# Performance work log

Hardware: AMD Instinct MI355X
Metric: run time of the kernel (lower is better)

## Reference

```python
import jax, jax.numpy as jnp
import numpy as np

B, S, HID = 2, 2048, 2048
NH, NKV, D = 16, 4, 128  # heads, kv heads, dim_per_head
ROPE_BASE = 10000.0


def setup_inputs() -> dict:
    key = jax.random.key(0)
    ks = jax.random.split(key, 5)
    x = jax.random.normal(ks[0], (B, S, HID), jnp.float32)
    wq = jax.random.normal(ks[1], (HID, NH * D), jnp.float32) * 0.02
    wk = jax.random.normal(ks[2], (HID, NKV * D), jnp.float32) * 0.02
    wv = jax.random.normal(ks[3], (HID, NKV * D), jnp.float32) * 0.02
    wo = jax.random.normal(ks[4], (NH * D, HID), jnp.float32) * 0.02
    inv_freq = 1.0 / (ROPE_BASE ** (jnp.arange(0, D, 2, dtype=jnp.float32) / D))
    freqs = jnp.outer(jnp.arange(S, dtype=jnp.float32), inv_freq)  # [S, D/2]
    cos, sin = jnp.cos(freqs), jnp.sin(freqs)
    mask = jnp.tril(jnp.ones((S, S), dtype=bool))  # causal, True = attend
    return {"x": x, "wq": wq, "wk": wk, "wv": wv, "wo": wo,
            "cos": cos, "sin": sin, "mask": mask}


def _rope_interleave(t, cos, sin):
    # t: [B, H, S, D]; cos/sin: [S, D/2]; interleaved pairs (even, odd)
    te, to = t[..., ::2], t[..., 1::2]
    c, s = cos[None, None], sin[None, None]
    re = te * c - to * s
    ro = to * c + te * s
    return jnp.stack([re, ro], axis=-1).reshape(t.shape)


def reference(x, wq, wk, wv, wo, cos, sin, mask):
    b, s, _ = x.shape
    # QKV projections + shape(): [B, S, hid] -> [B, H, S, D]
    q = (x @ wq).reshape(b, s, NH, D).transpose(0, 2, 1, 3)
    k = (x @ wk).reshape(b, s, NKV, D).transpose(0, 2, 1, 3)
    v = (x @ wv).reshape(b, s, NKV, D).transpose(0, 2, 1, 3)
    q = _rope_interleave(q, cos, sin)
    k = _rope_interleave(k, cos, sin)
    # GQA: repeat each kv head heads//heads_kv times consecutively
    rep = NH // NKV
    k = jnp.repeat(k, rep, axis=1)
    v = jnp.repeat(v, rep, axis=1)
    scores = jnp.einsum('bhqd,bhkd->bhqk', q, k) * (D ** -0.5)
    scores = scores.astype(jnp.float32)
    scores = jnp.where(mask[None, None], scores, jnp.finfo(jnp.float32).min)
    attn = jax.nn.softmax(scores, axis=-1).astype(x.dtype)
    ctx = jnp.einsum('bhqk,bhkd->bhqd', attn, v)
    ctx = ctx.transpose(0, 2, 1, 3).reshape(b, s, NH * D)  # unshape()
    return ctx @ wo
```

## Files before the change

### kernel.cpp

```cpp
#include <hip/hip_runtime.h>
#include <hip/hip_bf16.h>
#include <math.h>

#define S_LEN 2048
#define HIDW 2048
#define NHEAD 16
#define NKVH 4
#define HD 128
#define NB 2
#define MROWS (NB * S_LEN)
#define QKVN (NHEAD * HD + 2 * NKVH * HD)
#define KOFF (NHEAD * HD)
#define VOFF (NHEAD * HD + NKVH * HD)

typedef __bf16 bf16_t;
typedef __bf16 bf16x4_t __attribute__((ext_vector_type(4)));
typedef __bf16 bf16x8_t __attribute__((ext_vector_type(8)));
typedef float f32x4_t __attribute__((ext_vector_type(4)));

__device__ __forceinline__ void gload_lds16(const bf16_t* g, bf16_t* l) {
  __builtin_amdgcn_global_load_lds(
      (const __attribute__((address_space(1))) void*)g,
      (__attribute__((address_space(3))) void*)l, 16, 0, 0);
}

__device__ __forceinline__ f32x4_t zero4() {
  f32x4_t z = {0.f, 0.f, 0.f, 0.f};
  return z;
}

__device__ __forceinline__ float fexp2(float x) {
#if __has_builtin(__builtin_amdgcn_exp2f)
  return __builtin_amdgcn_exp2f(x);
#else
  return exp2f(x);
#endif
}

__global__ __launch_bounds__(256) void k_cvt8(const float* __restrict__ in,
                                              bf16_t* __restrict__ out, int n8) {
  int i = blockIdx.x * 256 + threadIdx.x;
  if (i >= n8) return;
  const float4* p = (const float4*)(in + (size_t)i * 8);
  float4 a = p[0], b = p[1];
  bf16x8_t r;
  r[0] = (bf16_t)a.x; r[1] = (bf16_t)a.y; r[2] = (bf16_t)a.z; r[3] = (bf16_t)a.w;
  r[4] = (bf16_t)b.x; r[5] = (bf16_t)b.y; r[6] = (bf16_t)b.z; r[7] = (bf16_t)b.w;
  *(bf16x8_t*)(out + (size_t)i * 8) = r;
}

__global__ __launch_bounds__(256) void k_tr_cvt(const float* __restrict__ in,
                                                bf16_t* __restrict__ out, int R, int C) {
  __shared__ float t[32][33];
  int c0 = blockIdx.x * 32, r0 = blockIdx.y * 32;
  int tx = threadIdx.x & 31, ty = threadIdx.x >> 5;
#pragma unroll
  for (int rr = ty; rr < 32; rr += 8) t[rr][tx] = in[(size_t)(r0 + rr) * C + c0 + tx];
  __syncthreads();
#pragma unroll
  for (int rr = ty; rr < 32; rr += 8)
    out[(size_t)(c0 + rr) * R + r0 + tx] = (bf16_t)t[tx][rr];
}

template <int EPI, int BMH>
__global__ __launch_bounds__(512, 2) void k_gemm256(const bf16_t* __restrict__ A,
                                                    const bf16_t* __restrict__ Bt,
                                                    void* __restrict__ Cout,
                                                    int M, int N, int K, int nby,
                                                    const float* __restrict__ cosT,
                                                    const float* __restrict__ sinT) {
  __shared__ bf16_t As[2][BMH * 128 * 64];
  __shared__ bf16_t Bs[2][256 * 64];

  int tid = threadIdx.x;
  int lane = tid & 63, wid = tid >> 6;
  int l15 = lane & 15, lg = lane >> 4;
  int wrb = (wid >> 2) * (BMH * 64);
  int wcb = (wid & 3) * 64;

  int nwg = gridDim.x;
  int qx = nwg >> 3;
  int lin = blockIdx.x;
  int wg = (lin & 7) * qx + (lin >> 3);
  int row0 = (wg / nby) * (BMH * 128), col0 = (wg % nby) * 256;

  int srow = tid >> 3;
  int scol = ((tid & 7) ^ (srow & 7)) * 8;
  const bf16_t* Ag = A + (size_t)(row0 + srow) * K + scol;
  const bf16_t* Bg = Bt + (size_t)(col0 + srow) * K + scol;

  f32x4_t acc[BMH * 4][4];
#pragma unroll
  for (int i = 0; i < BMH * 4; i++)
#pragma unroll
    for (int j = 0; j < 4; j++) acc[i][j] = zero4();

  int xr = (l15 & 7) << 4;
  int nk = K >> 6;

  auto stA = [&](int tt, int u) {
    gload_lds16(Ag + (size_t)u * 64 * K + (size_t)tt * 64,
                As[tt & 1] + u * 4096 + tid * 8);
  };
  auto stB = [&](int tt, int u) {
    gload_lds16(Bg + (size_t)u * 64 * K + (size_t)tt * 64,
                Bs[tt & 1] + u * 4096 + tid * 8);
  };

  for (int tt = 0; tt < 2 && tt < nk; tt++) {
    for (int u = 0; u < BMH * 2; u++) stA(tt, u);
    for (int u = 0; u < 4; u++) stB(tt, u);
  }
  if (nk > 1) {
    if constexpr (BMH == 2) asm volatile("s_waitcnt vmcnt(8)" ::: "memory");
    else asm volatile("s_waitcnt vmcnt(6)" ::: "memory");
  } else {
    asm volatile("s_waitcnt vmcnt(0)" ::: "memory");
  }
  __builtin_amdgcn_s_barrier();
  __builtin_amdgcn_sched_barrier(0);

  for (int t = 0; t < nk; t++) {
    int cur = t & 1;
    const char* Ac = (const char*)As[cur];
    const char* Bc = (const char*)Bs[cur];
    bool pf = (t + 2 < nk);

    bf16x8_t af0[4][2], bfr[4][2];
#pragma unroll
    for (int i = 0; i < 4; i++) {
      int row = wrb + i * 16 + l15;
#pragma unroll
      for (int kk = 0; kk < 2; kk++)
        af0[i][kk] = *(const bf16x8_t*)(Ac + ((row * 128 + kk * 64 + lg * 16) ^ xr));
    }
#pragma unroll
    for (int jn = 0; jn < 4; jn++) {
      int rowb = wcb + jn * 16 + l15;
#pragma unroll
      for (int kk = 0; kk < 2; kk++)
        bfr[jn][kk] = *(const bf16x8_t*)(Bc + ((rowb * 128 + kk * 64 + lg * 16) ^ xr));
    }
    __builtin_amdgcn_s_barrier();
    __builtin_amdgcn_s_setprio(1);
    if constexpr (BMH == 2) {
#pragma unroll
      for (int i = 0; i < 4; i++)
#pragma unroll
        for (int j = 0; j < 2; j++)
#pragma unroll
          for (int kk = 0; kk < 2; kk++)
            acc[i][j] = __builtin_amdgcn_mfma_f32_16x16x32_bf16(af0[i][kk], bfr[j][kk],
                                                                acc[i][j], 0, 0, 0);
    } else {
#pragma unroll
      for (int i = 0; i < 4; i++)
#pragma unroll
        for (int kk = 0; kk < 2; kk++)
          acc[i][0] = __builtin_amdgcn_mfma_f32_16x16x32_bf16(af0[i][kk], bfr[0][kk],
                                                              acc[i][0], 0, 0, 0);
    }
    __builtin_amdgcn_s_setprio(0);

    if (pf) {
      stA(t + 2, 0);
      if constexpr (BMH == 2) stA(t + 2, 2);
      else stA(t + 2, 1);
    }
    __builtin_amdgcn_s_barrier();
    __builtin_amdgcn_s_setprio(1);
    if constexpr (BMH == 2) {
#pragma unroll
      for (int i = 0; i < 4; i++)
#pragma unroll
        for (int j = 0; j < 2; j++)
#pragma unroll
          for (int kk = 0; kk < 2; kk++)
            acc[i][2 + j] = __builtin_amdgcn_mfma_f32_16x16x32_bf16(
                af0[i][kk], bfr[2 + j][kk], acc[i][2 + j], 0, 0, 0);
    } else {
#pragma unroll
      for (int i = 0; i < 4; i++)
#pragma unroll
        for (int kk = 0; kk < 2; kk++)
          acc[i][1] = __builtin_amdgcn_mfma_f32_16x16x32_bf16(af0[i][kk], bfr[1][kk],
                                                              acc[i][1], 0, 0, 0);
    }
    __builtin_amdgcn_s_setprio(0);

    bf16x8_t af1[4][2];
    if constexpr (BMH == 2) {
#pragma unroll
      for (int i = 0; i < 4; i++) {
        int row = wrb + 64 + i * 16 + l15;
#pragma unroll
        for (int kk = 0; kk < 2; kk++)
          af1[i][kk] = *(const bf16x8_t*)(Ac + ((row * 128 + kk * 64 + lg * 16) ^ xr));
      }
    }
    if (pf) { stB(t + 2, 0); stB(t + 2, 1); }
    __builtin_amdgcn_s_barrier();
    __builtin_amdgcn_s_setprio(1);
    if constexpr (BMH == 2) {
#pragma unroll
      for (int i = 0; i < 4; i++)
#pragma unroll
        for (int j = 0; j < 2; j++)
#pragma unroll
          for (int kk = 0; kk < 2; kk++)
            acc[4 + i][j] = __builtin_amdgcn_mfma_f32_16x16x32_bf16(
                af1[i][kk], bfr[j][kk], acc[4 + i][j], 0, 0, 0);
    } else {
#pragma unroll
      for (int i = 0; i < 4; i++)
#pragma unroll
        for (int kk = 0; kk < 2; kk++)
          acc[i][2] = __builtin_amdgcn_mfma_f32_16x16x32_bf16(af0[i][kk], bfr[2][kk],
                                                              acc[i][2], 0, 0, 0);
    }
    __builtin_amdgcn_s_setprio(0);

    if (pf) {
      stB(t + 2, 2); stB(t + 2, 3);
      if constexpr (BMH == 2) { stA(t + 2, 1); stA(t + 2, 3); }
    }
    __builtin_amdgcn_s_barrier();
    __builtin_amdgcn_s_setprio(1);
    if constexpr (BMH == 2) {
#pragma unroll
      for (int i = 0; i < 4; i++)
#pragma unroll
        for (int j = 0; j < 2; j++)
#pragma unroll
          for (int kk = 0; kk < 2; kk++)
            acc[4 + i][2 + j] = __builtin_amdgcn_mfma_f32_16x16x32_bf16(
                af1[i][kk], bfr[2 + j][kk], acc[4 + i][2 + j], 0, 0, 0);
    } else {
#pragma unroll
      for (int i = 0; i < 4; i++)
#pragma unroll
        for (int kk = 0; kk < 2; kk++)
          acc[i][3] = __builtin_amdgcn_mfma_f32_16x16x32_bf16(af0[i][kk], bfr[3][kk],
                                                              acc[i][3], 0, 0, 0);
    }
    __builtin_amdgcn_s_setprio(0);

    if (t + 1 < nk) {
      if (pf) {
        if constexpr (BMH == 2) asm volatile("s_waitcnt vmcnt(8)" ::: "memory");
        else asm volatile("s_waitcnt vmcnt(6)" ::: "memory");
      } else {
        asm volatile("s_waitcnt vmcnt(0)" ::: "memory");
      }
    }
    __builtin_amdgcn_s_barrier();
    __builtin_amdgcn_sched_barrier(0);
  }

  if (EPI == 2) {
    if (col0 < VOFF) {
      int sbase = row0 & (S_LEN - 1);
      bf16_t* cosL = &As[0][0];
      bf16_t* sinL = &Bs[0][0];
#pragma unroll
      for (int k = 0; k < 8; k++) {
        gload_lds16((const bf16_t*)(cosT + (size_t)sbase * 64 + k * 2048 + tid * 4),
                    cosL + k * 4096 + tid * 8);
        gload_lds16((const bf16_t*)(sinT + (size_t)sbase * 64 + k * 2048 + tid * 4),
                    sinL + k * 4096 + tid * 8);
      }
      asm volatile("s_waitcnt vmcnt(0)" ::: "memory");
      __builtin_amdgcn_s_barrier();
      const float* cosF = (const float*)cosL;
      const float* sinF = (const float*)sinL;
      const float QS = 0.08838834764831845f * 1.4426950408889634f;
#pragma unroll
      for (int i = 0; i < BMH * 4; i++) {
#pragma unroll
        for (int j = 0; j < 4; j++) {
          int c = col0 + wcb + j * 16 + l15;
          int rlb = wrb + i * 16 + lg * 4;
          float scale = (c < KOFF) ? QS : 1.0f;
          int p0 = (c & 127) >> 1;
          int codd = c & 1;
#pragma unroll
          for (int qd = 0; qd < 4; qd++) {
            int rl = rlb + qd;
            float self = acc[i][j][qd];
            float other = __shfl_xor(self, 1);
            float cv = cosF[rl * 64 + p0], sv = sinF[rl * 64 + p0];
            float outv = codd ? (self * cv + other * sv) : (self * cv - other * sv);
            ((bf16_t*)Cout)[(size_t)(row0 + rl) * N + c] = (bf16_t)(outv * scale);
          }
        }
      }
    } else {
#pragma unroll
      for (int i = 0; i < BMH * 4; i++) {
#pragma unroll
        for (int j = 0; j < 4; j++) {
          int r = row0 + wrb + i * 16 + lg * 4;
          int c = col0 + wcb + j * 16 + l15;
#pragma unroll
          for (int qd = 0; qd < 4; qd++)
            ((bf16_t*)Cout)[(size_t)(r + qd) * N + c] = (bf16_t)acc[i][j][qd];
        }
      }
    }
  } else {
#pragma unroll
    for (int i = 0; i < BMH * 4; i++) {
#pragma unroll
      for (int j = 0; j < 4; j++) {
        int r = row0 + wrb + i * 16 + lg * 4;
        int c = col0 + wcb + j * 16 + l15;
#pragma unroll
        for (int qd = 0; qd < 4; qd++)
          ((float*)Cout)[(size_t)(r + qd) * N + c] = acc[i][j][qd];
      }
    }
  }
}

__global__ __launch_bounds__(256) void k_vt(const bf16_t* __restrict__ qkv,
                                            bf16_t* __restrict__ vt) {
  __shared__ bf16_t t[32][33];
  int s0 = blockIdx.x * 32;
  int dt = (blockIdx.y & 3) * 32;
  int h = blockIdx.y >> 2;
  int b = blockIdx.z;
  int tx = threadIdx.x & 31, ty = threadIdx.x >> 5;
#pragma unroll
  for (int rr = ty; rr < 32; rr += 8)
    t[rr][tx] = qkv[(size_t)(b * S_LEN + s0 + rr) * QKVN + VOFF + h * HD + dt + tx];
  __syncthreads();
#pragma unroll
  for (int rr = ty; rr < 32; rr += 8)
    vt[((size_t)((b * NKVH + h) * HD + dt + rr)) * S_LEN + s0 + tx] = t[tx][rr];
}

__global__ __launch_bounds__(256, 2) void k_attn(const bf16_t* __restrict__ qkv,
                                                 const bf16_t* __restrict__ vt,
                                                 bf16_t* __restrict__ ctx) {
  __shared__ bf16_t Ks[2 * 64 * 128];
  __shared__ bf16_t Vs[2 * 128 * 64];
  __shared__ bf16_t plds[4][16 * 72];

  int tid = threadIdx.x;
  int lane = tid & 63, wid = tid >> 6;
  int idx = blockIdx.x;
  int bh = idx & 31;
  int qg = 31 - (idx >> 5);
  int b = bh >> 4, h = bh & 15;
  int kvh = h >> 2;
  int q0 = qg * 64 + wid * 16;
  int l15 = lane & 15, lg = lane >> 4;

  const bf16_t* Kbase = qkv + (size_t)(b * S_LEN) * QKVN + KOFF + kvh * HD;
  const bf16_t* Vbase = vt + (size_t)(b * NKVH + kvh) * HD * S_LEN;

  const bf16_t* Qp = qkv + (size_t)(b * S_LEN + q0 + l15) * QKVN + h * HD + lg * 8;
  bf16x8_t aq[4];
#pragma unroll
  for (int kk = 0; kk < 4; kk++) aq[kk] = *(const bf16x8_t*)(Qp + kk * 32);

  int Ls[4], Lk[4], Lv[4];
#pragma unroll
  for (int u = 0; u < 4; u++) {
    int L = u * 4096 + tid * 16;
    Ls[u] = L >> 1;
    Lk[u] = L ^ (((L >> 8) & 7) << 4);
    Lv[u] = L ^ (((L >> 7) & 7) << 4);
  }

  f32x4_t o[8];
#pragma unroll
  for (int j = 0; j < 8; j++) o[j] = zero4();
  float ms = -INFINITY, lsum = 0.f;

  bf16_t* pbuf = &plds[wid][0];
  int xr = (l15 & 7) << 4;
  int ntiles = qg + 1;
  int qcol = q0 + l15;

#pragma unroll
  for (int u = 0; u < 4; u++) {
    gload_lds16(Kbase + (size_t)(Lk[u] >> 8) * QKVN + ((Lk[u] & 255) >> 1), Ks + Ls[u]);
    gload_lds16(Vbase + (size_t)(Lv[u] >> 7) * S_LEN + ((Lv[u] & 127) >> 1), Vs + Ls[u]);
  }
  __syncthreads();

  for (int t = 0; t < ntiles; t++) {
    int kv0 = t * 64;
    if (t + 1 < ntiles) {
      const bf16_t* Kn = Kbase + (size_t)(kv0 + 64) * QKVN;
      const bf16_t* Vn = Vbase + kv0 + 64;
      int bo = ((t + 1) & 1) * 8192;
#pragma unroll
      for (int u = 0; u < 4; u++) {
        gload_lds16(Kn + (size_t)(Lk[u] >> 8) * QKVN + ((Lk[u] & 255) >> 1), Ks + bo + Ls[u]);
        gload_lds16(Vn + (size_t)(Lv[u] >> 7) * S_LEN + ((Lv[u] & 127) >> 1), Vs + bo + Ls[u]);
      }
    }
    const char* Kb = (const char*)Ks + (t & 1) * 16384;
    const char* Vb = (const char*)Vs + (t & 1) * 16384;

    f32x4_t sacc[4];
#pragma unroll
    for (int cg = 0; cg < 4; cg++) sacc[cg] = zero4();
#pragma unroll
    for (int cg = 0; cg < 4; cg++) {
#pragma unroll
      for (int kk = 0; kk < 4; kk++) {
        int boff = ((cg * 16 + l15) * 256 + kk * 64 + lg * 16) ^ xr;
        bf16x8_t bk = *(const bf16x8_t*)(Kb + boff);
        sacc[cg] = __builtin_amdgcn_mfma_f32_16x16x32_bf16(bk, aq[kk], sacc[cg], 0, 0, 0);
      }
    }
    if (kv0 + 63 > q0) {
#pragma unroll
      for (int cg = 0; cg < 4; cg++) {
#pragma unroll
        for (int i = 0; i < 4; i++) {
          int kvg = kv0 + cg * 16 + lg * 4 + i;
          if (kvg > qcol) sacc[cg][i] = -1e30f;
        }
      }
    }
    float pmax = sacc[0][0];
#pragma unroll
    for (int cg = 0; cg < 4; cg++)
#pragma unroll
      for (int i = 0; i < 4; i++) pmax = fmaxf(pmax, sacc[cg][i]);
    pmax = fmaxf(pmax, __shfl_xor(pmax, 16));
    pmax = fmaxf(pmax, __shfl_xor(pmax, 32));
    if (__any(pmax - ms > 8.0f)) {
      float nm = fmaxf(ms, pmax);
      float sc = fexp2(ms - nm);
      ms = nm;
      lsum *= sc;
      float sci[4];
#pragma unroll
      for (int i = 0; i < 4; i++) sci[i] = __shfl(sc, lg * 4 + i);
#pragma unroll
      for (int j = 0; j < 8; j++)
#pragma unroll
        for (int i = 0; i < 4; i++) o[j][i] *= sci[i];
    }
    float ls = 0.f;
#pragma unroll
    for (int cg = 0; cg < 4; cg++)
#pragma unroll
      for (int i = 0; i < 4; i++) {
        sacc[cg][i] = fexp2(sacc[cg][i] - ms);
        ls += sacc[cg][i];
      }
    ls += __shfl_xor(ls, 16);
    ls += __shfl_xor(ls, 32);
    lsum += ls;
#pragma unroll
    for (int cg = 0; cg < 4; cg++)
#pragma unroll
      for (int i = 0; i < 4; i++)
        pbuf[l15 * 72 + cg * 16 + lg * 4 + i] = (bf16_t)sacc[cg][i];
    __builtin_amdgcn_wave_barrier();
    bf16x8_t pa0 = *(const bf16x8_t*)(pbuf + l15 * 72 + lg * 8);
    bf16x8_t pa1 = *(const bf16x8_t*)(pbuf + l15 * 72 + 32 + lg * 8);
    __builtin_amdgcn_wave_barrier();
#pragma unroll
    for (int j = 0; j < 8; j++) {
      int d = j * 16 + l15;
      int bo0 = (d * 128 + lg * 16) ^ xr;
      int bo1 = (d * 128 + 64 + lg * 16) ^ xr;
      o[j] = __builtin_amdgcn_mfma_f32_16x16x32_bf16(
          pa0, *(const bf16x8_t*)(Vb + bo0), o[j], 0, 0, 0);
      o[j] = __builtin_amdgcn_mfma_f32_16x16x32_bf16(
          pa1, *(const bf16x8_t*)(Vb + bo1), o[j], 0, 0, 0);
    }
    __syncthreads();
  }

  bf16_t* Cp = ctx + (size_t)(b * S_LEN + q0) * KOFF + h * HD;
#pragma unroll
  for (int i = 0; i < 4; i++) {
    float inv = 1.f / __shfl(lsum, lg * 4 + i);
    int row = lg * 4 + i;
#pragma unroll
    for (int j = 0; j < 8; j++)
      Cp[(size_t)row * KOFF + j * 16 + l15] = (bf16_t)(o[j][i] * inv);
  }
}

extern "C" void kernel_launch(void* const* d_in, const int* in_sizes, int n_in,
                              void* d_out, int out_size, void* d_ws, size_t ws_size,
                              hipStream_t stream) {
  const float* x = (const float*)d_in[0];
  const float* wq = (const float*)d_in[1];
  const float* wk = (const float*)d_in[2];
  const float* wv = (const float*)d_in[3];
  const float* wo = (const float*)d_in[4];
  const float* cosT = (const float*)d_in[5];
  const float* sinT = (const float*)d_in[6];

  bf16_t* xb = (bf16_t*)d_ws;
  bf16_t* wqkvT = xb + (size_t)MROWS * HIDW;
  bf16_t* woT = wqkvT + (size_t)QKVN * HIDW;
  bf16_t* qkv = woT + (size_t)HIDW * HIDW;
  bf16_t* vtb = qkv + (size_t)MROWS * QKVN;

  k_cvt8<<<MROWS * HIDW / 8 / 256, 256, 0, stream>>>(x, xb, MROWS * HIDW / 8);
  k_tr_cvt<<<dim3(KOFF / 32, HIDW / 32), 256, 0, stream>>>(wq, wqkvT, HIDW, KOFF);
  k_tr_cvt<<<dim3((NKVH * HD) / 32, HIDW / 32), 256, 0, stream>>>(
      wk, wqkvT + (size_t)KOFF * HIDW, HIDW, NKVH * HD);
  k_tr_cvt<<<dim3((NKVH * HD) / 32, HIDW / 32), 256, 0, stream>>>(
      wv, wqkvT + (size_t)VOFF * HIDW, HIDW, NKVH * HD);
  k_tr_cvt<<<dim3(HIDW / 32, KOFF / 32), 256, 0, stream>>>(wo, woT, KOFF, HIDW);
  k_gemm256<2, 2><<<(MROWS / 256) * (QKVN / 256), 512, 0, stream>>>(
      xb, wqkvT, qkv, MROWS, QKVN, HIDW, QKVN / 256, cosT, sinT);
  k_vt<<<dim3(S_LEN / 32, 4 * NKVH, NB), 256, 0, stream>>>(qkv, vtb);
  k_attn<<<32 * 32, 256, 0, stream>>>(qkv, vtb, xb);
  k_gemm256<0, 1><<<(MROWS / 128) * (HIDW / 256), 512, 0, stream>>>(
      xb, woT, d_out, MROWS, HIDW, KOFF, HIDW / 256, nullptr, nullptr);
}
```

Before: 193.9 us.

## Simplify GEMM mainloop to single-stage prefetch with one barrier per tile

Replaces the depth-two prefetch, whose global-to-LDS loads were interleaved between four barrier-separated MFMA phases, with a simpler depth-one scheme. All loads for the next K tile are issued at the top of each iteration into the other LDS buffer, and the loop waits with vmcnt(0) plus one barrier at the end. B fragments are now read from LDS in two halves just before they are used, which lowers register pressure and removes three barriers per iteration. In exchange there is less latency hiding, because only one tile is in flight and every iteration fully drains outstanding memory loads. The sched_barrier hints are also removed, leaving scheduling to the compiler.

New measurement: 214.6 us. +10.7%, slower.

```diff
diff --git a/kernel.cpp b/kernel.cpp
--- a/kernel.cpp
+++ b/kernel.cpp
@@ -107,26 +107,22 @@
                 Bs[tt & 1] + u * 4096 + tid * 8);
   };
 
-  for (int tt = 0; tt < 2 && tt < nk; tt++) {
-    for (int u = 0; u < BMH * 2; u++) stA(tt, u);
-    for (int u = 0; u < 4; u++) stB(tt, u);
-  }
-  if (nk > 1) {
-    if constexpr (BMH == 2) asm volatile("s_waitcnt vmcnt(8)" ::: "memory");
-    else asm volatile("s_waitcnt vmcnt(6)" ::: "memory");
-  } else {
-    asm volatile("s_waitcnt vmcnt(0)" ::: "memory");
-  }
+  for (int u = 0; u < BMH * 2; u++) stA(0, u);
+  for (int u = 0; u < 4; u++) stB(0, u);
+  asm volatile("s_waitcnt vmcnt(0)" ::: "memory");
   __builtin_amdgcn_s_barrier();
-  __builtin_amdgcn_sched_barrier(0);
 
   for (int t = 0; t < nk; t++) {
-    int cur = t & 1;
-    const char* Ac = (const char*)As[cur];
-    const char* Bc = (const char*)Bs[cur];
-    bool pf = (t + 2 < nk);
-
-    bf16x8_t af0[4][2], bfr[4][2];
+    const char* Ac = (const char*)As[t & 1];
+    const char* Bc = (const char*)Bs[t & 1];
+    if (t + 1 < nk) {
+#pragma unroll
+      for (int u = 0; u < BMH * 2; u++) stA(t + 1, u);
+#pragma unroll
+      for (int u = 0; u < 4; u++) stB(t + 1, u);
+    }
+
+    bf16x8_t af0[4][2], b01[2][2];
 #pragma unroll
     for (int i = 0; i < 4; i++) {
       int row = wrb + i * 16 + l15;
@@ -135,61 +131,44 @@
         af0[i][kk] = *(const bf16x8_t*)(Ac + ((row * 128 + kk * 64 + lg * 16) ^ xr));
     }
 #pragma unroll
-    for (int jn = 0; jn < 4; jn++) {
-      int rowb = wcb + jn * 16 + l15;
+    for (int j = 0; j < 2; j++) {
+      int rowb = wcb + j * 16 + l15;
 #pragma unroll
       for (int kk = 0; kk < 2; kk++)
-        bfr[jn][kk] = *(const bf16x8_t*)(Bc + ((rowb * 128 + kk * 64 + lg * 16) ^ xr));
-    }
-    __builtin_amdgcn_s_barrier();
+        b01[j][kk] = *(const bf16x8_t*)(Bc + ((rowb * 128 + kk * 64 + lg * 16) ^ xr));
+    }
     __builtin_amdgcn_s_setprio(1);
+#pragma unroll
+    for (int i = 0; i < 4; i++)
+#pragma unroll
+      for (int j = 0; j < 2; j++)
+#pragma unroll
+        for (int kk = 0; kk < 2; kk++)
+          acc[i][j] = __builtin_amdgcn_mfma_f32_16x16x32_bf16(af0[i][kk], b01[j][kk],
+                                                              acc[i][j], 0, 0, 0);
+    __builtin_amdgcn_s_setprio(0);
+
+    bf16x8_t b23[2][2];
+#pragma unroll
+    for (int j = 0; j < 2; j++) {
+      int rowb = wcb + (2 + j) * 16 + l15;
+#pragma unroll
+      for (int kk = 0; kk < 2; kk++)
+        b23[j][kk] = *(const bf16x8_t*)(Bc + ((rowb * 128 + kk * 64 + lg * 16) ^ xr));
+    }
+    __builtin_amdgcn_s_setprio(1);
+#pragma unroll
+    for (int i = 0; i < 4; i++)
+#pragma unroll
+      for (int j = 0; j < 2; j++)
+#pragma unroll
+        for (int kk = 0; kk < 2; kk++)
+          acc[i][2 + j] = __builtin_amdgcn_mfma_f32_16x16x32_bf16(
+              af0[i][kk], b23[j][kk], acc[i][2 + j], 0, 0, 0);
+    __builtin_amdgcn_s_setprio(0);
+
     if constexpr (BMH == 2) {
-#pragma unroll
-      for (int i = 0; i < 4; i++)
-#pragma unroll
-        for (int j = 0; j < 2; j++)
-#pragma unroll
-          for (int kk = 0; kk < 2; kk++)
-            acc[i][j] = __builtin_amdgcn_mfma_f32_16x16x32_bf16(af0[i][kk], bfr[j][kk],
-                                                                acc[i][j], 0, 0, 0);
-    } else {
-#pragma unroll
-      for (int i = 0; i < 4; i++)
-#pragma unroll
-        for (int kk = 0; kk < 2; kk++)
-          acc[i][0] = __builtin_amdgcn_mfma_f32_16x16x32_bf16(af0[i][kk], bfr[0][kk],
-                                                              acc[i][0], 0, 0, 0);
-    }
-    __builtin_amdgcn_s_setprio(0);
-
-    if (pf) {
-      stA(t + 2, 0);
-      if constexpr (BMH == 2) stA(t + 2, 2);
-      else stA(t + 2, 1);
-    }
-    __builtin_amdgcn_s_barrier();
-    __builtin_amdgcn_s_setprio(1);
-    if constexpr (BMH == 2) {
-#pragma unroll
-      for (int i = 0; i < 4; i++)
-#pragma unroll
-        for (int j = 0; j < 2; j++)
-#pragma unroll
-          for (int kk = 0; kk < 2; kk++)
-            acc[i][2 + j] = __builtin_amdgcn_mfma_f32_16x16x32_bf16(
-                af0[i][kk], bfr[2 + j][kk], acc[i][2 + j], 0, 0, 0);
-    } else {
-#pragma unroll
-      for (int i = 0; i < 4; i++)
-#pragma unroll
-        for (int kk = 0; kk < 2; kk++)
-          acc[i][1] = __builtin_amdgcn_mfma_f32_16x16x32_bf16(af0[i][kk], bfr[1][kk],
-                                                              acc[i][1], 0, 0, 0);
-    }
-    __builtin_amdgcn_s_setprio(0);
-
-    bf16x8_t af1[4][2];
-    if constexpr (BMH == 2) {
+      bf16x8_t af1[4][2];
 #pragma unroll
       for (int i = 0; i < 4; i++) {
         int row = wrb + 64 + i * 16 + l15;
@@ -197,11 +176,7 @@
         for (int kk = 0; kk < 2; kk++)
           af1[i][kk] = *(const bf16x8_t*)(Ac + ((row * 128 + kk * 64 + lg * 16) ^ xr));
       }
-    }
-    if (pf) { stB(t + 2, 0); stB(t + 2, 1); }
-    __builtin_amdgcn_s_barrier();
-    __builtin_amdgcn_s_setprio(1);
-    if constexpr (BMH == 2) {
+      __builtin_amdgcn_s_setprio(1);
 #pragma unroll
       for (int i = 0; i < 4; i++)
 #pragma unroll
@@ -209,24 +184,7 @@
 #pragma unroll
           for (int kk = 0; kk < 2; kk++)
             acc[4 + i][j] = __builtin_amdgcn_mfma_f32_16x16x32_bf16(
-                af1[i][kk], bfr[j][kk], acc[4 + i][j], 0, 0, 0);
-    } else {
-#pragma unroll
-      for (int i = 0; i < 4; i++)
-#pragma unroll
-        for (int kk = 0; kk < 2; kk++)
-          acc[i][2] = __builtin_amdgcn_mfma_f32_16x16x32_bf16(af0[i][kk], bfr[2][kk],
-                                                              acc[i][2], 0, 0, 0);
-    }
-    __builtin_amdgcn_s_setprio(0);
-
-    if (pf) {
-      stB(t + 2, 2); stB(t + 2, 3);
-      if constexpr (BMH == 2) { stA(t + 2, 1); stA(t + 2, 3); }
-    }
-    __builtin_amdgcn_s_barrier();
-    __builtin_amdgcn_s_setprio(1);
-    if constexpr (BMH == 2) {
+                af1[i][kk], b01[j][kk], acc[4 + i][j], 0, 0, 0);
 #pragma unroll
       for (int i = 0; i < 4; i++)
 #pragma unroll
@@ -234,27 +192,12 @@
 #pragma unroll
           for (int kk = 0; kk < 2; kk++)
             acc[4 + i][2 + j] = __builtin_amdgcn_mfma_f32_16x16x32_bf16(
-                af1[i][kk], bfr[2 + j][kk], acc[4 + i][2 + j], 0, 0, 0);
-    } else {
-#pragma unroll
-      for (int i = 0; i < 4; i++)
-#pragma unroll
-        for (int kk = 0; kk < 2; kk++)
-          acc[i][3] = __builtin_amdgcn_mfma_f32_16x16x32_bf16(af0[i][kk], bfr[3][kk],
-                                                              acc[i][3], 0, 0, 0);
-    }
-    __builtin_amdgcn_s_setprio(0);
-
-    if (t + 1 < nk) {
-      if (pf) {
-        if constexpr (BMH == 2) asm volatile("s_waitcnt vmcnt(8)" ::: "memory");
-        else asm volatile("s_waitcnt vmcnt(6)" ::: "memory");
-      } else {
-        asm volatile("s_waitcnt vmcnt(0)" ::: "memory");
-      }
-    }
+                af1[i][kk], b23[j][kk], acc[4 + i][2 + j], 0, 0, 0);
+      __builtin_amdgcn_s_setprio(0);
+    }
+
+    if (t + 1 < nk) asm volatile("s_waitcnt vmcnt(0)" ::: "memory");
     __builtin_amdgcn_s_barrier();
-    __builtin_amdgcn_sched_barrier(0);
   }
 
   if (EPI == 2) {
```

## Use 256x192 tiles for QKV GEMM and specialize output GEMM kernel

Applied to the files above, without the earlier changes.

Retiles the fused QKV projection GEMM to 256x192 blocks so the grid yields 256 workgroups, matching the CU count for better occupancy balance instead of 192 blocks. The RoPE epilogue is reworked to handle mixed Q/K/V column tiles and to stage cos/sin in two row halves through LDS. The output projection GEMM is split into its own non-templated kernel with constant dimensions. Narrower tiles lower per-block arithmetic intensity and add epilogue branching.

New measurement: 201.4 us. +3.9%, slower.

```diff
diff --git a/kernel.cpp b/kernel.cpp
--- a/kernel.cpp
+++ b/kernel.cpp
@@ -14,7 +14,6 @@
 #define VOFF (NHEAD * HD + NKVH * HD)
 
 typedef __bf16 bf16_t;
-typedef __bf16 bf16x4_t __attribute__((ext_vector_type(4)));
 typedef __bf16 bf16x8_t __attribute__((ext_vector_type(8)));
 typedef float f32x4_t __attribute__((ext_vector_type(4)));
 
@@ -62,71 +61,61 @@
     out[(size_t)(c0 + rr) * R + r0 + tx] = (bf16_t)t[tx][rr];
 }
 
-template <int EPI, int BMH>
-__global__ __launch_bounds__(512, 2) void k_gemm256(const bf16_t* __restrict__ A,
-                                                    const bf16_t* __restrict__ Bt,
-                                                    void* __restrict__ Cout,
-                                                    int M, int N, int K, int nby,
-                                                    const float* __restrict__ cosT,
-                                                    const float* __restrict__ sinT) {
-  __shared__ bf16_t As[2][BMH * 128 * 64];
-  __shared__ bf16_t Bs[2][256 * 64];
-
+__global__ __launch_bounds__(512, 2) void k_gemm_qkv(const bf16_t* __restrict__ A,
+                                                     const bf16_t* __restrict__ Bt,
+                                                     bf16_t* __restrict__ qkv,
+                                                     const float* __restrict__ cosT,
+                                                     const float* __restrict__ sinT) {
+  __shared__ bf16_t As[2][256 * 64];
+  __shared__ bf16_t Bs[2][192 * 64];
+  const int K = HIDW;
   int tid = threadIdx.x;
   int lane = tid & 63, wid = tid >> 6;
   int l15 = lane & 15, lg = lane >> 4;
-  int wrb = (wid >> 2) * (BMH * 64);
-  int wcb = (wid & 3) * 64;
+  int wrb = (wid >> 2) * 128;
+  int wcb = (wid & 3) * 48;
 
   int nwg = gridDim.x;
   int qx = nwg >> 3;
   int lin = blockIdx.x;
   int wg = (lin & 7) * qx + (lin >> 3);
-  int row0 = (wg / nby) * (BMH * 128), col0 = (wg % nby) * 256;
+  int row0 = (wg >> 4) * 256, col0 = (wg & 15) * 192;
 
   int srow = tid >> 3;
   int scol = ((tid & 7) ^ (srow & 7)) * 8;
   const bf16_t* Ag = A + (size_t)(row0 + srow) * K + scol;
   const bf16_t* Bg = Bt + (size_t)(col0 + srow) * K + scol;
 
-  f32x4_t acc[BMH * 4][4];
-#pragma unroll
-  for (int i = 0; i < BMH * 4; i++)
-#pragma unroll
-    for (int j = 0; j < 4; j++) acc[i][j] = zero4();
+  f32x4_t acc[8][3];
+#pragma unroll
+  for (int i = 0; i < 8; i++)
+#pragma unroll
+    for (int j = 0; j < 3; j++) acc[i][j] = zero4();
 
   int xr = (l15 & 7) << 4;
-  int nk = K >> 6;
+  const int nk = K >> 6;
 
   auto stA = [&](int tt, int u) {
-    gload_lds16(Ag + (size_t)u * 64 * K + (size_t)tt * 64,
-                As[tt & 1] + u * 4096 + tid * 8);
+    gload_lds16(Ag + (size_t)u * 64 * K + (size_t)tt * 64, As[tt & 1] + u * 4096 + tid * 8);
   };
   auto stB = [&](int tt, int u) {
-    gload_lds16(Bg + (size_t)u * 64 * K + (size_t)tt * 64,
-                Bs[tt & 1] + u * 4096 + tid * 8);
+    gload_lds16(Bg + (size_t)u * 64 * K + (size_t)tt * 64, Bs[tt & 1] + u * 4096 + tid * 8);
   };
 
-  for (int tt = 0; tt < 2 && tt < nk; tt++) {
-    for (int u = 0; u < BMH * 2; u++) stA(tt, u);
-    for (int u = 0; u < 4; u++) stB(tt, u);
-  }
-  if (nk > 1) {
-    if constexpr (BMH == 2) asm volatile("s_waitcnt vmcnt(8)" ::: "memory");
-    else asm volatile("s_waitcnt vmcnt(6)" ::: "memory");
-  } else {
-    asm volatile("s_waitcnt vmcnt(0)" ::: "memory");
-  }
+  for (int tt = 0; tt < 2; tt++) {
+    for (int u = 0; u < 4; u++) stA(tt, u);
+    for (int u = 0; u < 3; u++) stB(tt, u);
+  }
+  asm volatile("s_waitcnt vmcnt(7)" ::: "memory");
   __builtin_amdgcn_s_barrier();
   __builtin_amdgcn_sched_barrier(0);
 
   for (int t = 0; t < nk; t++) {
-    int cur = t & 1;
-    const char* Ac = (const char*)As[cur];
-    const char* Bc = (const char*)Bs[cur];
+    const char* Ac = (const char*)As[t & 1];
+    const char* Bc = (const char*)Bs[t & 1];
     bool pf = (t + 2 < nk);
 
-    bf16x8_t af0[4][2], bfr[4][2];
+    bf16x8_t af0[4][2], bfr[3][2];
 #pragma unroll
     for (int i = 0; i < 4; i++) {
       int row = wrb + i * 16 + l15;
@@ -135,189 +124,267 @@
         af0[i][kk] = *(const bf16x8_t*)(Ac + ((row * 128 + kk * 64 + lg * 16) ^ xr));
     }
 #pragma unroll
-    for (int jn = 0; jn < 4; jn++) {
-      int rowb = wcb + jn * 16 + l15;
-#pragma unroll
-      for (int kk = 0; kk < 2; kk++)
-        bfr[jn][kk] = *(const bf16x8_t*)(Bc + ((rowb * 128 + kk * 64 + lg * 16) ^ xr));
-    }
-    __builtin_amdgcn_s_barrier();
-    __builtin_amdgcn_s_setprio(1);
-    if constexpr (BMH == 2) {
-#pragma unroll
-      for (int i = 0; i < 4; i++)
-#pragma unroll
-        for (int j = 0; j < 2; j++)
-#pragma unroll
-          for (int kk = 0; kk < 2; kk++)
-            acc[i][j] = __builtin_amdgcn_mfma_f32_16x16x32_bf16(af0[i][kk], bfr[j][kk],
-                                                                acc[i][j], 0, 0, 0);
-    } else {
-#pragma unroll
-      for (int i = 0; i < 4; i++)
+    for (int j = 0; j < 3; j++) {
+      int rowb = wcb + j * 16 + l15;
+#pragma unroll
+      for (int kk = 0; kk < 2; kk++)
+        bfr[j][kk] = *(const bf16x8_t*)(Bc + ((rowb * 128 + kk * 64 + lg * 16) ^ xr));
+    }
+    __builtin_amdgcn_s_barrier();
+    __builtin_amdgcn_s_setprio(1);
+#pragma unroll
+    for (int i = 0; i < 4; i++)
+#pragma unroll
+      for (int j = 0; j < 2; j++)
 #pragma unroll
         for (int kk = 0; kk < 2; kk++)
-          acc[i][0] = __builtin_amdgcn_mfma_f32_16x16x32_bf16(af0[i][kk], bfr[0][kk],
-                                                              acc[i][0], 0, 0, 0);
-    }
-    __builtin_amdgcn_s_setprio(0);
-
-    if (pf) {
-      stA(t + 2, 0);
-      if constexpr (BMH == 2) stA(t + 2, 2);
-      else stA(t + 2, 1);
-    }
-    __builtin_amdgcn_s_barrier();
-    __builtin_amdgcn_s_setprio(1);
-    if constexpr (BMH == 2) {
-#pragma unroll
-      for (int i = 0; i < 4; i++)
-#pragma unroll
-        for (int j = 0; j < 2; j++)
-#pragma unroll
-          for (int kk = 0; kk < 2; kk++)
-            acc[i][2 + j] = __builtin_amdgcn_mfma_f32_16x16x32_bf16(
-                af0[i][kk], bfr[2 + j][kk], acc[i][2 + j], 0, 0, 0);
-    } else {
-#pragma unroll
-      for (int i = 0; i < 4; i++)
+          acc[i][j] = __builtin_amdgcn_mfma_f32_16x16x32_bf16(af0[i][kk], bfr[j][kk],
+                                                              acc[i][j], 0, 0, 0);
+    __builtin_amdgcn_s_setprio(0);
+
+    if (pf) { stA(t + 2, 0); stA(t + 2, 2); }
+    __builtin_amdgcn_s_barrier();
+    __builtin_amdgcn_s_setprio(1);
+#pragma unroll
+    for (int i = 0; i < 4; i++)
+#pragma unroll
+      for (int kk = 0; kk < 2; kk++)
+        acc[i][2] = __builtin_amdgcn_mfma_f32_16x16x32_bf16(af0[i][kk], bfr[2][kk],
+                                                            acc[i][2], 0, 0, 0);
+    __builtin_amdgcn_s_setprio(0);
+
+    bf16x8_t af1[4][2];
+#pragma unroll
+    for (int i = 0; i < 4; i++) {
+      int row = wrb + 64 + i * 16 + l15;
+#pragma unroll
+      for (int kk = 0; kk < 2; kk++)
+        af1[i][kk] = *(const bf16x8_t*)(Ac + ((row * 128 + kk * 64 + lg * 16) ^ xr));
+    }
+    if (pf) { stB(t + 2, 0); stB(t + 2, 1); }
+    __builtin_amdgcn_s_barrier();
+    __builtin_amdgcn_s_setprio(1);
+#pragma unroll
+    for (int i = 0; i < 4; i++)
+#pragma unroll
+      for (int j = 0; j < 2; j++)
 #pragma unroll
         for (int kk = 0; kk < 2; kk++)
-          acc[i][1] = __builtin_amdgcn_mfma_f32_16x16x32_bf16(af0[i][kk], bfr[1][kk],
-                                                              acc[i][1], 0, 0, 0);
-    }
-    __builtin_amdgcn_s_setprio(0);
-
-    bf16x8_t af1[4][2];
-    if constexpr (BMH == 2) {
-#pragma unroll
-      for (int i = 0; i < 4; i++) {
-        int row = wrb + 64 + i * 16 + l15;
-#pragma unroll
-        for (int kk = 0; kk < 2; kk++)
-          af1[i][kk] = *(const bf16x8_t*)(Ac + ((row * 128 + kk * 64 + lg * 16) ^ xr));
-      }
-    }
-    if (pf) { stB(t + 2, 0); stB(t + 2, 1); }
-    __builtin_amdgcn_s_barrier();
-    __builtin_amdgcn_s_setprio(1);
-    if constexpr (BMH == 2) {
-#pragma unroll
-      for (int i = 0; i < 4; i++)
-#pragma unroll
-        for (int j = 0; j < 2; j++)
-#pragma unroll
-          for (int kk = 0; kk < 2; kk++)
-            acc[4 + i][j] = __builtin_amdgcn_mfma_f32_16x16x32_bf16(
-                af1[i][kk], bfr[j][kk], acc[4 + i][j], 0, 0, 0);
-    } else {
-#pragma unroll
-      for (int i = 0; i < 4; i++)
-#pragma unroll
-        for (int kk = 0; kk < 2; kk++)
-          acc[i][2] = __builtin_amdgcn_mfma_f32_16x16x32_bf16(af0[i][kk], bfr[2][kk],
-                                                              acc[i][2], 0, 0, 0);
-    }
-    __builtin_amdgcn_s_setprio(0);
-
-    if (pf) {
-      stB(t + 2, 2); stB(t + 2, 3);
-      if constexpr (BMH == 2) { stA(t + 2, 1); stA(t + 2, 3); }
-    }
-    __builtin_amdgcn_s_barrier();
-    __builtin_amdgcn_s_setprio(1);
-    if constexpr (BMH == 2) {
-#pragma unroll
-      for (int i = 0; i < 4; i++)
-#pragma unroll
-        for (int j = 0; j < 2; j++)
-#pragma unroll
-          for (int kk = 0; kk < 2; kk++)
-            acc[4 + i][2 + j] = __builtin_amdgcn_mfma_f32_16x16x32_bf16(
-                af1[i][kk], bfr[2 + j][kk], acc[4 + i][2 + j], 0, 0, 0);
-    } else {
-#pragma unroll
-      for (int i = 0; i < 4; i++)
-#pragma unroll
-        for (int kk = 0; kk < 2; kk++)
-          acc[i][3] = __builtin_amdgcn_mfma_f32_16x16x32_bf16(af0[i][kk], bfr[3][kk],
-                                                              acc[i][3], 0, 0, 0);
-    }
+          acc[4 + i][j] = __builtin_amdgcn_mfma_f32_16x16x32_bf16(
+              af1[i][kk], bfr[j][kk], acc[4 + i][j], 0, 0, 0);
+    __builtin_amdgcn_s_setprio(0);
+
+    if (pf) { stB(t + 2, 2); stA(t + 2, 1); stA(t + 2, 3); }
+    __builtin_amdgcn_s_barrier();
+    __builtin_amdgcn_s_setprio(1);
+#pragma unroll
+    for (int i = 0; i < 4; i++)
+#pragma unroll
+      for (int kk = 0; kk < 2; kk++)
+        acc[4 + i][2] = __builtin_amdgcn_mfma_f32_16x16x32_bf16(
+            af1[i][kk], bfr[2][kk], acc[4 + i][2], 0, 0, 0);
     __builtin_amdgcn_s_setprio(0);
 
     if (t + 1 < nk) {
-      if (pf) {
-        if constexpr (BMH == 2) asm volatile("s_waitcnt vmcnt(8)" ::: "memory");
-        else asm volatile("s_waitcnt vmcnt(6)" ::: "memory");
-      } else {
-        asm volatile("s_waitcnt vmcnt(0)" ::: "memory");
-      }
+      if (pf) asm volatile("s_waitcnt vmcnt(7)" ::: "memory");
+      else    asm volatile("s_waitcnt vmcnt(0)" ::: "memory");
     }
     __builtin_amdgcn_s_barrier();
     __builtin_amdgcn_sched_barrier(0);
   }
 
-  if (EPI == 2) {
-    if (col0 < VOFF) {
-      int sbase = row0 & (S_LEN - 1);
-      bf16_t* cosL = &As[0][0];
-      bf16_t* sinL = &Bs[0][0];
-#pragma unroll
-      for (int k = 0; k < 8; k++) {
-        gload_lds16((const bf16_t*)(cosT + (size_t)sbase * 64 + k * 2048 + tid * 4),
-                    cosL + k * 4096 + tid * 8);
-        gload_lds16((const bf16_t*)(sinT + (size_t)sbase * 64 + k * 2048 + tid * 4),
-                    sinL + k * 4096 + tid * 8);
+  if (col0 < VOFF) {
+    int sbase = row0 & (S_LEN - 1);
+    const float QS = 0.08838834764831845f * 1.4426950408889634f;
+#pragma unroll
+    for (int hh = 0; hh < 2; hh++) {
+      const float* cp = cosT + (size_t)(sbase + hh * 128) * 64;
+      const float* sp = sinT + (size_t)(sbase + hh * 128) * 64;
+#pragma unroll
+      for (int k = 0; k < 4; k++) {
+        gload_lds16((const bf16_t*)(cp + k * 2048 + (size_t)tid * 4),
+                    As[0] + k * 4096 + tid * 8);
+        gload_lds16((const bf16_t*)(sp + k * 2048 + (size_t)tid * 4),
+                    As[1] + k * 4096 + tid * 8);
       }
       asm volatile("s_waitcnt vmcnt(0)" ::: "memory");
       __builtin_amdgcn_s_barrier();
-      const float* cosF = (const float*)cosL;
-      const float* sinF = (const float*)sinL;
-      const float QS = 0.08838834764831845f * 1.4426950408889634f;
-#pragma unroll
-      for (int i = 0; i < BMH * 4; i++) {
-#pragma unroll
-        for (int j = 0; j < 4; j++) {
-          int c = col0 + wcb + j * 16 + l15;
-          int rlb = wrb + i * 16 + lg * 4;
-          float scale = (c < KOFF) ? QS : 1.0f;
-          int p0 = (c & 127) >> 1;
-          int codd = c & 1;
-#pragma unroll
-          for (int qd = 0; qd < 4; qd++) {
-            int rl = rlb + qd;
-            float self = acc[i][j][qd];
-            float other = __shfl_xor(self, 1);
-            float cv = cosF[rl * 64 + p0], sv = sinF[rl * 64 + p0];
-            float outv = codd ? (self * cv + other * sv) : (self * cv - other * sv);
-            ((bf16_t*)Cout)[(size_t)(row0 + rl) * N + c] = (bf16_t)(outv * scale);
+      if ((wrb >> 7) == hh) {
+        const float* cosF = (const float*)As[0];
+        const float* sinF = (const float*)As[1];
+#pragma unroll
+        for (int i = 0; i < 8; i++) {
+#pragma unroll
+          for (int j = 0; j < 3; j++) {
+            int c = col0 + wcb + j * 16 + l15;
+            int rll = i * 16 + lg * 4;
+            if (c < VOFF) {
+              float scale = (c < KOFF) ? QS : 1.0f;
+              int p0 = (c & 127) >> 1;
+              int codd = c & 1;
+#pragma unroll
+              for (int qd = 0; qd < 4; qd++) {
+                float self = acc[i][j][qd];
+                float other = __shfl_xor(self, 1);
+                float cv = cosF[(rll + qd) * 64 + p0], sv = sinF[(rll + qd) * 64 + p0];
+                float outv = codd ? (self * cv + other * sv) : (self * cv - other * sv);
+                qkv[(size_t)(row0 + hh * 128 + rll + qd) * QKVN + c] =
+                    (bf16_t)(outv * scale);
+              }
+            } else {
+#pragma unroll
+              for (int qd = 0; qd < 4; qd++)
+                qkv[(size_t)(row0 + hh * 128 + rll + qd) * QKVN + c] =
+                    (bf16_t)acc[i][j][qd];
+            }
           }
         }
       }
-    } else {
-#pragma unroll
-      for (int i = 0; i < BMH * 4; i++) {
-#pragma unroll
-        for (int j = 0; j < 4; j++) {
-          int r = row0 + wrb + i * 16 + lg * 4;
-          int c = col0 + wcb + j * 16 + l15;
-#pragma unroll
-          for (int qd = 0; qd < 4; qd++)
-            ((bf16_t*)Cout)[(size_t)(r + qd) * N + c] = (bf16_t)acc[i][j][qd];
-        }
-      }
+      __builtin_amdgcn_s_barrier();
     }
   } else {
 #pragma unroll
-    for (int i = 0; i < BMH * 4; i++) {
-#pragma unroll
-      for (int j = 0; j < 4; j++) {
+    for (int i = 0; i < 8; i++) {
+#pragma unroll
+      for (int j = 0; j < 3; j++) {
         int r = row0 + wrb + i * 16 + lg * 4;
         int c = col0 + wcb + j * 16 + l15;
 #pragma unroll
         for (int qd = 0; qd < 4; qd++)
-          ((float*)Cout)[(size_t)(r + qd) * N + c] = acc[i][j][qd];
-      }
+          qkv[(size_t)(r + qd) * QKVN + c] = (bf16_t)acc[i][j][qd];
+      }
+    }
+  }
+}
+
+__global__ __launch_bounds__(512, 2) void k_gemm_out(const bf16_t* __restrict__ A,
+                                                     const bf16_t* __restrict__ Bt,
+                                                     float* __restrict__ Cout) {
+  __shared__ bf16_t As[2][128 * 64];
+  __shared__ bf16_t Bs[2][256 * 64];
+  const int K = KOFF;
+  const int N = HIDW;
+  int tid = threadIdx.x;
+  int lane = tid & 63, wid = tid >> 6;
+  int l15 = lane & 15, lg = lane >> 4;
+  int wrb = (wid >> 2) * 64;
+  int wcb = (wid & 3) * 64;
+
+  int nwg = gridDim.x;
+  int qx = nwg >> 3;
+  int lin = blockIdx.x;
+  int wg = (lin & 7) * qx + (lin >> 3);
+  int row0 = (wg >> 3) * 128, col0 = (wg & 7) * 256;
+
+  int srow = tid >> 3;
+  int scol = ((tid & 7) ^ (srow & 7)) * 8;
+  const bf16_t* Ag = A + (size_t)(row0 + srow) * K + scol;
+  const bf16_t* Bg = Bt + (size_t)(col0 + srow) * K + scol;
+
+  f32x4_t acc[4][4];
+#pragma unroll
+  for (int i = 0; i < 4; i++)
+#pragma unroll
+    for (int j = 0; j < 4; j++) acc[i][j] = zero4();
+
+  int xr = (l15 & 7) << 4;
+  const int nk = K >> 6;
+
+  auto stA = [&](int tt, int u) {
+    gload_lds16(Ag + (size_t)u * 64 * K + (size_t)tt * 64, As[tt & 1] + u * 4096 + tid * 8);
+  };
+  auto stB = [&](int tt, int u) {
+    gload_lds16(Bg + (size_t)u * 64 * K + (size_t)tt * 64, Bs[tt & 1] + u * 4096 + tid * 8);
+  };
+
+  for (int tt = 0; tt < 2; tt++) {
+    for (int u = 0; u < 2; u++) stA(tt, u);
+    for (int u = 0; u < 4; u++) stB(tt, u);
+  }
+  asm volatile("s_waitcnt vmcnt(6)" ::: "memory");
+  __builtin_amdgcn_s_barrier();
+  __builtin_amdgcn_sched_barrier(0);
+
+  for (int t = 0; t < nk; t++) {
+    const char* Ac = (const char*)As[t & 1];
+    const char* Bc = (const char*)Bs[t & 1];
+    bool pf = (t + 2 < nk);
+
+    bf16x8_t af0[4][2], bfr[4][2];
+#pragma unroll
+    for (int i = 0; i < 4; i++) {
+      int row = wrb + i * 16 + l15;
+#pragma unroll
+      for (int kk = 0; kk < 2; kk++)
+        af0[i][kk] = *(const bf16x8_t*)(Ac + ((row * 128 + kk * 64 + lg * 16) ^ xr));
+    }
+#pragma unroll
+    for (int j = 0; j < 4; j++) {
+      int rowb = wcb + j * 16 + l15;
+#pragma unroll
+      for (int kk = 0; kk < 2; kk++)
+        bfr[j][kk] = *(const bf16x8_t*)(Bc + ((rowb * 128 + kk * 64 + lg * 16) ^ xr));
+    }
+    __builtin_amdgcn_s_barrier();
+    __builtin_amdgcn_s_setprio(1);
+#pragma unroll
+    for (int i = 0; i < 4; i++)
+#pragma unroll
+      for (int kk = 0; kk < 2; kk++)
+        acc[i][0] = __builtin_amdgcn_mfma_f32_16x16x32_bf16(af0[i][kk], bfr[0][kk],
+                                                            acc[i][0], 0, 0, 0);
+    __builtin_amdgcn_s_setprio(0);
+
+    if (pf) { stA(t + 2, 0); stA(t + 2, 1); }
+    __builtin_amdgcn_s_barrier();
+    __builtin_amdgcn_s_setprio(1);
+#pragma unroll
+    for (int i = 0; i < 4; i++)
+#pragma unroll
+      for (int kk = 0; kk < 2; kk++)
+        acc[i][1] = __builtin_amdgcn_mfma_f32_16x16x32_bf16(af0[i][kk], bfr[1][kk],
+                                                            acc[i][1], 0, 0, 0);
+    __builtin_amdgcn_s_setprio(0);
+
+    if (pf) { stB(t + 2, 0); stB(t + 2, 1); }
+    __builtin_amdgcn_s_barrier();
+    __builtin_amdgcn_s_setprio(1);
+#pragma unroll
+    for (int i = 0; i < 4; i++)
+#pragma unroll
+      for (int kk = 0; kk < 2; kk++)
+        acc[i][2] = __builtin_amdgcn_mfma_f32_16x16x32_bf16(af0[i][kk], bfr[2][kk],
+                                                            acc[i][2], 0, 0, 0);
+    __builtin_amdgcn_s_setprio(0);
+
+    if (pf) { stB(t + 2, 2); stB(t + 2, 3); }
+    __builtin_amdgcn_s_barrier();
+    __builtin_amdgcn_s_setprio(1);
+#pragma unroll
+    for (int i = 0; i < 4; i++)
+#pragma unroll
+      for (int kk = 0; kk < 2; kk++)
+        acc[i][3] = __builtin_amdgcn_mfma_f32_16x16x32_bf16(af0[i][kk], bfr[3][kk],
+                                                            acc[i][3], 0, 0, 0);
+    __builtin_amdgcn_s_setprio(0);
+
+    if (t + 1 < nk) {
+      if (pf) asm volatile("s_waitcnt vmcnt(6)" ::: "memory");
+      else    asm volatile("s_waitcnt vmcnt(0)" ::: "memory");
+    }
+    __builtin_amdgcn_s_barrier();
+    __builtin_amdgcn_sched_barrier(0);
+  }
+
+#pragma unroll
+  for (int i = 0; i < 4; i++) {
+#pragma unroll
+    for (int j = 0; j < 4; j++) {
+      int r = row0 + wrb + i * 16 + lg * 4;
+      int c = col0 + wcb + j * 16 + l15;
+#pragma unroll
+      for (int qd = 0; qd < 4; qd++)
+        Cout[(size_t)(r + qd) * N + c] = acc[i][j][qd];
     }
   }
 }
@@ -515,10 +582,10 @@
   k_tr_cvt<<<dim3((NKVH * HD) / 32, HIDW / 32), 256, 0, stream>>>(
       wv, wqkvT + (size_t)VOFF * HIDW, HIDW, NKVH * HD);
   k_tr_cvt<<<dim3(HIDW / 32, KOFF / 32), 256, 0, stream>>>(wo, woT, KOFF, HIDW);
-  k_gemm256<2, 2><<<(MROWS / 256) * (QKVN / 256), 512, 0, stream>>>(
-      xb, wqkvT, qkv, MROWS, QKVN, HIDW, QKVN / 256, cosT, sinT);
+  k_gemm_qkv<<<(MROWS / 256) * (QKVN / 192), 512, 0, stream>>>(
+      xb, wqkvT, qkv, cosT, sinT);
   k_vt<<<dim3(S_LEN / 32, 4 * NKVH, NB), 256, 0, stream>>>(qkv, vtb);
   k_attn<<<32 * 32, 256, 0, stream>>>(qkv, vtb, xb);
-  k_gemm256<0, 1><<<(MROWS / 128) * (HIDW / 256), 512, 0, stream>>>(
-      xb, woT, d_out, MROWS, HIDW, KOFF, HIDW / 256, nullptr, nullptr);
-}
+  k_gemm_out<<<(MROWS / 128) * (HIDW / 256), 512, 0, stream>>>(xb, woT,
+                                                               (float*)d_out);
+}
```
